# Optimization experiments

Hardware: AMD Instinct MI355X
Metric: run time of the kernel (lower is better)

## Reference

```python
import jax, jax.numpy as jnp
import numpy as np

NUM_HEADS = 8
ROPE_BASE = 10000.0


def _rope_cache(T, D, dtype=jnp.float32):
    # LLaMA-style rope cache: cos/sin of shape [T, D]
    inv_freq = 1.0 / (ROPE_BASE ** (jnp.arange(0, D, 2, dtype=dtype) / D))
    t = jnp.arange(T, dtype=dtype)
    freqs = t[:, None] * inv_freq[None, :]            # [T, D/2]
    emb = jnp.concatenate([freqs, freqs], axis=-1)    # [T, D]
    return jnp.cos(emb), jnp.sin(emb)


def _rotate_half(x):
    x1, x2 = jnp.split(x, 2, axis=-1)
    return jnp.concatenate([-x2, x1], axis=-1)


def setup_inputs() -> dict:
    key = jax.random.key(0)
    k1, k2, k3 = jax.random.split(key, 3)
    B, T, C = 4, 2048, 512
    x = jax.random.normal(k1, (B, T, C), dtype=jnp.float32)
    Wqkv = jax.random.normal(k2, (C, 3 * C), dtype=jnp.float32) * (1.0 / np.sqrt(C))
    Wproj = jax.random.normal(k3, (C, C), dtype=jnp.float32) * (1.0 / np.sqrt(C))
    return {"x": x, "Wqkv": Wqkv, "Wproj": Wproj}


def reference(x, Wqkv, Wproj):
    B, T, C = x.shape
    H = NUM_HEADS
    D = C // H

    qkv = jnp.einsum('btc,cf->btf', x, Wqkv)          # [B,T,3C]
    qkv = qkv.reshape(B, T, H, 3 * D)
    q, k, v = jnp.split(qkv, 3, axis=-1)              # each [B,T,H,D]
    q = q.transpose(0, 2, 1, 3)                       # [B,H,T,D]
    k = k.transpose(0, 2, 1, 3)
    v = v.transpose(0, 2, 1, 3)

    cos, sin = _rope_cache(T, D, dtype=x.dtype)       # [T,D]
    cos = cos[None, None, :, :]
    sin = sin[None, None, :, :]
    q = q * cos + _rotate_half(q) * sin
    k = k * cos + _rotate_half(k) * sin

    scale = 1.0 / np.sqrt(D)
    scores = jnp.einsum('bhqd,bhkd->bhqk', q, k) * scale  # [B,H,T,T]
    causal = jnp.tril(jnp.ones((T, T), dtype=bool))
    scores = jnp.where(causal[None, None, :, :], scores, jnp.finfo(scores.dtype).min)
    attn = jax.nn.softmax(scores, axis=-1)
    out = jnp.einsum('bhqk,bhkd->bhqd', attn, v)      # [B,H,T,D]
    out = out.transpose(0, 2, 1, 3).reshape(B, T, C)
    return jnp.einsum('btc,cd->btd', out, Wproj)
```

## Files before the change

kernel.cpp:

```cpp
#include <hip/hip_runtime.h>
#include <hip/hip_bf16.h>
#include <stdint.h>

constexpr int Bn = 4;
constexpr int Tn = 2048;
constexpr int Cn = 512;
constexpr int Hn = 8;
constexpr int Dn = 64;
constexpr int BT = Bn * Tn;
constexpr int NQKV = 3 * Cn;

typedef __attribute__((ext_vector_type(4))) float  f32x4;
typedef __attribute__((ext_vector_type(8))) short  s16x8;
typedef __attribute__((ext_vector_type(4))) short  s16x4;

__device__ __forceinline__ short f2bs(float f) {
    __hip_bfloat16 h = __float2bfloat16(f);
    return *reinterpret_cast<short*>(&h);
}

__device__ __forceinline__ void gload16(const short* g, short* l) {
    __builtin_amdgcn_global_load_lds(
        (const __attribute__((address_space(1))) void*)g,
        (__attribute__((address_space(3))) void*)l, 16, 0, 0);
}


__global__ __launch_bounds__(256) void k_conv_x(const float* __restrict__ x,
                                                short* __restrict__ xb) {
    int i = blockIdx.x * 256 + threadIdx.x;
    f32x4 v = reinterpret_cast<const f32x4*>(x)[i];
    s16x4 o;
    o[0] = f2bs(v[0]); o[1] = f2bs(v[1]); o[2] = f2bs(v[2]); o[3] = f2bs(v[3]);
    reinterpret_cast<s16x4*>(xb)[i] = o;
}

__global__ __launch_bounds__(256) void k_wTt(const float* __restrict__ Wqkv,
                                             const float* __restrict__ Wproj,
                                             short* __restrict__ wqkvT,
                                             short* __restrict__ wprojT) {
    int bid = blockIdx.x;
    const float* W; short* out; int N, n0, k0;
    if (bid < 192) {
        W = Wqkv; out = wqkvT; N = NQKV;
        n0 = (bid >> 3) * 64; k0 = (bid & 7) * 64;
    } else {
        bid -= 192;
        W = Wproj; out = wprojT; N = Cn;
        n0 = (bid >> 3) * 64; k0 = (bid & 7) * 64;
    }
    __shared__ float lds[64 * 65];
    const int tid = threadIdx.x;
#pragma unroll
    for (int i = 0; i < 16; ++i) {
        int flat = i * 256 + tid;
        int k = flat >> 6, n = flat & 63;
        lds[n * 65 + k] = W[(size_t)(k0 + k) * N + n0 + n];
    }
    __syncthreads();
#pragma unroll
    for (int i = 0; i < 16; ++i) {
        int flat = i * 256 + tid;
        int n = flat >> 6, k = flat & 63;
        out[(size_t)(n0 + n) * 512 + k0 + k] = f2bs(lds[n * 65 + k]);
    }
}

__global__ __launch_bounds__(256) void k_rope(float2* __restrict__ csT) {
    int i = blockIdx.x * 256 + threadIdx.x;
    int t = i >> 6, d = i & 63;
    float inv = exp2f(-(float)(d & 31) * 0.41524101186f);
    float fr = (float)t * inv;
    csT[i] = make_float2(cosf(fr), sinf(fr));
}


template <int MODE>
__global__ __launch_bounds__(256, 2) void gemm_kernel(
    const short* __restrict__ A, const short* __restrict__ Bt,
    const float2* __restrict__ csT,
    short* __restrict__ Qb, short* __restrict__ Kb, short* __restrict__ Vt,
    float* __restrict__ outF) {
    const int m0 = blockIdx.y * 128;
    const int n0 = blockIdx.x * 128;
    const int tid = threadIdx.x;
    const int w = tid >> 6, lane = tid & 63;
    const int qi = lane & 15, g = lane >> 4;
    const int wr = w >> 1, wc = w & 1;

    __shared__ short As[2][128 * 64];
    __shared__ short Bs[2][128 * 64];

    f32x4 acc[4][4];
#pragma unroll
    for (int mt = 0; mt < 4; ++mt)
#pragma unroll
        for (int nt = 0; nt < 4; ++nt) acc[mt][nt] = (f32x4){0.f, 0.f, 0.f, 0.f};

    const int lr = lane >> 3;
    const int lc = (lane & 7) ^ lr;

#define STAGEG(buf, k0)                                                         \
    {                                                                           \
        _Pragma("unroll")                                                       \
        for (int s4_ = 0; s4_ < 4; ++s4_) {                                     \
            int slot_ = s4_ * 4 + w;                                            \
            int r_ = slot_ * 8 + lr;                                            \
            gload16(&A[(size_t)(m0 + r_) * 512 + (k0) + lc * 8],                \
                    &As[buf][slot_ * 512 + lane * 8]);                          \
            gload16(&Bt[(size_t)(n0 + r_) * 512 + (k0) + lc * 8],               \
                    &Bs[buf][slot_ * 512 + lane * 8]);                          \
        }                                                                       \
    }

    STAGEG(0, 0);
    __syncthreads();

    for (int it = 0; it < 8; ++it) {
        if (it + 1 < 8) STAGEG((it + 1) & 1, (it + 1) * 64);
        const int cur = it & 1;
#pragma unroll
        for (int kk = 0; kk < 2; ++kk) {
            s16x8 af[4], bf[4];
#pragma unroll
            for (int mt = 0; mt < 4; ++mt) {
                int row = wr * 64 + mt * 16 + qi;
                af[mt] = *(const s16x8*)&As[cur][row * 64 + (((kk << 2) | g) ^ (qi & 7)) * 8];
            }
#pragma unroll
            for (int nt = 0; nt < 4; ++nt) {
                int row = wc * 64 + nt * 16 + qi;
                bf[nt] = *(const s16x8*)&Bs[cur][row * 64 + (((kk << 2) | g) ^ (qi & 7)) * 8];
            }
#pragma unroll
            for (int mt = 0; mt < 4; ++mt)
#pragma unroll
                for (int nt = 0; nt < 4; ++nt)
                    acc[mt][nt] = __builtin_amdgcn_mfma_f32_16x16x32_bf16(
                        af[mt], bf[nt], acc[mt][nt], 0, 0, 0);
        }
        __syncthreads();
    }
#undef STAGEG

    if (MODE == 1) {
#pragma unroll
        for (int mt = 0; mt < 4; ++mt)
#pragma unroll
            for (int nt = 0; nt < 4; ++nt)
#pragma unroll
                for (int r = 0; r < 4; ++r)
                    outF[(size_t)(m0 + wr * 64 + mt * 16 + 4 * g + r) * 512 +
                         n0 + wc * 64 + nt * 16 + qi] = acc[mt][nt][r];
    } else {
        const int seg64 = (n0 >> 6) + wc;
        const int h = seg64 / 3;
        const int seg = seg64 % 3;
        const int b = m0 >> 11;
        const int tb = (m0 & 2047) + wr * 64;
        const float QSC = 0.125f * 1.44269504f;
        if (seg == 2) {
            const size_t vbase = (size_t)(b * Hn + h) * Dn;
#pragma unroll
            for (int mt = 0; mt < 4; ++mt)
#pragma unroll
                for (int nt = 0; nt < 4; ++nt)
#pragma unroll
                    for (int r = 0; r < 4; ++r) {
                        int t = tb + mt * 16 + 4 * g + r;
                        int d = nt * 16 + qi;
                        int o = t & 31;
                        int jj = (t & ~31) + ((o >> 2) & 3) * 8 + (o >> 4) * 4 + (o & 3);
                        Vt[(vbase + d) * Tn + jj] = f2bs(acc[mt][nt][r]);
                    }
        } else {
            short* dst = (seg == 0) ? Qb : Kb;
            const float post = (seg == 0) ? QSC : 1.0f;
            const size_t headbase = (size_t)(b * Hn + h) * Tn;
#pragma unroll
            for (int mt = 0; mt < 4; ++mt)
#pragma unroll
                for (int nt = 0; nt < 4; ++nt)
#pragma unroll
                    for (int r = 0; r < 4; ++r) {
                        int t = tb + mt * 16 + 4 * g + r;
                        int d = nt * 16 + qi;
                        float val = acc[mt][nt][r];
                        float pv = (nt < 2) ? -acc[mt][nt + 2][r] : acc[mt][nt - 2][r];
                        float2 cs = csT[t * 64 + d];
                        dst[(headbase + t) * Dn + d] = f2bs((val * cs.x + pv * cs.y) * post);
                    }
        }
    }
}


__global__ __launch_bounds__(256, 4) void attn_kernel(const short* __restrict__ Qb,
                                                      const short* __restrict__ Kb,
                                                      const short* __restrict__ Vt,
                                                      short* __restrict__ AO) {
    const int idx = blockIdx.x;
    const int bh = idx & 31;
    const int qt = 31 - (idx >> 5);
    const int q0 = qt * 64;
    const int tid = threadIdx.x;
    const int w = tid >> 6, lane = tid & 63;
    const int qi = lane & 15, g = lane >> 4;
    const int b = bh >> 3, h = bh & 7;

    __shared__ short Ks[2][64 * 64];
    __shared__ short Vs[2][64 * 64];

    const short* Qh = Qb + (size_t)bh * Tn * Dn;
    const short* Kh = Kb + (size_t)bh * Tn * Dn;
    const short* Vh = Vt + (size_t)bh * Dn * Tn;

    const int wrow0 = q0 + w * 16;
    s16x8 qf[2];
#pragma unroll
    for (int dh = 0; dh < 2; ++dh)
        qf[dh] = *(const s16x8*)&Qh[(size_t)(wrow0 + qi) * Dn + dh * 32 + g * 8];

    f32x4 O[4];
#pragma unroll
    for (int dt = 0; dt < 4; ++dt) O[dt] = (f32x4){0.f, 0.f, 0.f, 0.f};
    float lsum = 0.f;

    const int nch = qt + 1;
    const f32x4 z4 = {0.f, 0.f, 0.f, 0.f};

    const int lr = lane >> 3;
    const int lc = (lane & 7) ^ lr;

#define STAGE(buf, ch)                                                          \
    {                                                                           \
        const int kv0_ = (ch) * 64;                                             \
        _Pragma("unroll")                                                       \
        for (int i_ = 0; i_ < 2; ++i_) {                                        \
            int slot_ = i_ * 4 + w;                                             \
            int r_ = slot_ * 8 + lr;                                            \
            gload16(&Kh[(size_t)(kv0_ + r_) * 64 + lc * 8],                     \
                    &Ks[buf][slot_ * 512 + lane * 8]);                          \
            gload16(&Vh[(size_t)r_ * Tn + kv0_ + lc * 8],                       \
                    &Vs[buf][slot_ * 512 + lane * 8]);                          \
        }                                                                       \
    }

    STAGE(0, 0);
    __syncthreads();

    for (int ch = 0; ch < nch; ++ch) {
        if (ch + 1 < nch) STAGE((ch + 1) & 1, ch + 1);
        const int kv0 = ch * 64;
        const int cur = ch & 1;

        f32x4 sacc[4];
#pragma unroll
        for (int sub = 0; sub < 4; ++sub) {
            const int krow = sub * 16 + qi;
            s16x8 ka = *(const s16x8*)&Ks[cur][krow * 64 + ((g ^ (qi & 7))) * 8];
            s16x8 kc = *(const s16x8*)&Ks[cur][krow * 64 + (((4 | g) ^ (qi & 7))) * 8];
            f32x4 t0 = __builtin_amdgcn_mfma_f32_16x16x32_bf16(ka, qf[0], z4, 0, 0, 0);
            sacc[sub] = __builtin_amdgcn_mfma_f32_16x16x32_bf16(kc, qf[1], t0, 0, 0, 0);
        }

        float pe[16];
        if (kv0 + 63 <= wrow0) {
#pragma unroll
            for (int e2 = 0; e2 < 16; ++e2)
                pe[e2] = exp2f(sacc[e2 >> 2][e2 & 3]);
        } else {
            const int qrow = wrow0 + qi;
#pragma unroll
            for (int sub = 0; sub < 4; ++sub)
#pragma unroll
                for (int r = 0; r < 4; ++r) {
                    int key = kv0 + sub * 16 + 4 * g + r;
                    pe[sub * 4 + r] = (key <= qrow) ? exp2f(sacc[sub][r]) : 0.f;
                }
        }
        {
            float a0 = (pe[0] + pe[1]) + (pe[2] + pe[3]);
            float a1 = (pe[4] + pe[5]) + (pe[6] + pe[7]);
            float a2 = (pe[8] + pe[9]) + (pe[10] + pe[11]);
            float a3 = (pe[12] + pe[13]) + (pe[14] + pe[15]);
            lsum += (a0 + a1) + (a2 + a3);
        }
        s16x8 pf[2];
#pragma unroll
        for (int c = 0; c < 2; ++c)
#pragma unroll
            for (int e2 = 0; e2 < 8; ++e2) pf[c][e2] = f2bs(pe[c * 8 + e2]);

#pragma unroll
        for (int c = 0; c < 2; ++c)
#pragma unroll
            for (int dt = 0; dt < 4; ++dt) {
                const int vrow = dt * 16 + qi;
                s16x8 vf = *(const s16x8*)&Vs[cur][vrow * 64 +
                                                   ((((c << 2) | g) ^ (qi & 7))) * 8];
                O[dt] = __builtin_amdgcn_mfma_f32_16x16x32_bf16(
                    pf[c], vf, O[dt], 0, 0, 0);
            }
        __syncthreads();
    }
#undef STAGE

    lsum += __shfl_xor(lsum, 16);
    lsum += __shfl_xor(lsum, 32);

#pragma unroll
    for (int r = 0; r < 4; ++r) {
        float li = __shfl(lsum, 4 * g + r);
        float inv = 1.f / li;
        int t = wrow0 + 4 * g + r;
#pragma unroll
        for (int dt = 0; dt < 4; ++dt)
            AO[((size_t)(b * Tn + t)) * Cn + h * 64 + dt * 16 + qi] =
                f2bs(O[dt][r] * inv);
    }
}


extern "C" void kernel_launch(void* const* d_in, const int* in_sizes, int n_in,
                              void* d_out, int out_size, void* d_ws, size_t ws_size,
                              hipStream_t stream) {
    const float* x = (const float*)d_in[0];
    const float* Wqkv = (const float*)d_in[1];
    const float* Wproj = (const float*)d_in[2];
    float* out = (float*)d_out;

    char* ws = (char*)d_ws;
    size_t o = 0;
    short* xb = (short*)(ws + o);      o += (size_t)BT * Cn * 2;
    short* wqkvT = (short*)(ws + o);   o += (size_t)NQKV * Cn * 2;
    short* wprojT = (short*)(ws + o);  o += (size_t)Cn * Cn * 2;
    short* Qb = (short*)(ws + o);      o += (size_t)Bn * Hn * Tn * Dn * 2;
    short* Kb = (short*)(ws + o);      o += (size_t)Bn * Hn * Tn * Dn * 2;
    short* Vt = (short*)(ws + o);      o += (size_t)Bn * Hn * Tn * Dn * 2;
    float2* csT = (float2*)(ws + o);   o += (size_t)Tn * Dn * 8;

    k_conv_x<<<BT * Cn / 4 / 256, 256, 0, stream>>>(x, xb);
    k_wTt<<<dim3(256), 256, 0, stream>>>(Wqkv, Wproj, wqkvT, wprojT);
    k_rope<<<Tn * Dn / 256, 256, 0, stream>>>(csT);

    gemm_kernel<0><<<dim3(NQKV / 128, BT / 128), 256, 0, stream>>>(
        xb, wqkvT, csT, Qb, Kb, Vt, nullptr);

    attn_kernel<<<dim3(1024), 256, 0, stream>>>(Qb, Kb, Vt, xb );

    gemm_kernel<1><<<dim3(Cn / 128, BT / 128), 256, 0, stream>>>(
        xb , wprojT, csT, nullptr, nullptr, nullptr, out);
}
```

Baseline: 93.73 us.

## Split KV chunks across warp pairs, with 32 query rows per warp and LDS reduction

The attention kernel now gives each warp 32 query rows, two 16-row subtiles, instead of 16. The four warps are split into two parity groups that handle alternating KV chunks. Each loaded K/V fragment from LDS is reused for two MFMAs, and warps skip chunks that lie fully past the causal diagonal of their rows. At the end, partial O accumulators and row sums from the odd-parity warps are reduced through shared memory before normalisation. This cuts LDS reads per MFMA and skips masked work, at the cost of more registers, half the warps idling on each chunk, and an extra reduction step.

```diff
diff --git a/kernel.cpp b/kernel.cpp
--- a/kernel.cpp
+++ b/kernel.cpp
@@ -206,6 +206,8 @@
     const int tid = threadIdx.x;
     const int w = tid >> 6, lane = tid & 63;
     const int qi = lane & 15, g = lane >> 4;
+    const int p = w & 1;
+    const int par = w >> 1;
     const int b = bh >> 3, h = bh & 7;
 
     __shared__ short Ks[2][64 * 64];
@@ -215,16 +217,21 @@
     const short* Kh = Kb + (size_t)bh * Tn * Dn;
     const short* Vh = Vt + (size_t)bh * Dn * Tn;
 
-    const int wrow0 = q0 + w * 16;
-    s16x8 qf[2];
-#pragma unroll
-    for (int dh = 0; dh < 2; ++dh)
-        qf[dh] = *(const s16x8*)&Qh[(size_t)(wrow0 + qi) * Dn + dh * 32 + g * 8];
-
-    f32x4 O[4];
-#pragma unroll
-    for (int dt = 0; dt < 4; ++dt) O[dt] = (f32x4){0.f, 0.f, 0.f, 0.f};
-    float lsum = 0.f;
+    const int wrow0 = q0 + p * 32;
+    s16x8 qf[2][2];
+#pragma unroll
+    for (int qs = 0; qs < 2; ++qs)
+#pragma unroll
+        for (int dh = 0; dh < 2; ++dh)
+            qf[qs][dh] = *(const s16x8*)&Qh[(size_t)(wrow0 + qs * 16 + qi) * Dn +
+                                            dh * 32 + g * 8];
+
+    f32x4 O[2][4];
+#pragma unroll
+    for (int qs = 0; qs < 2; ++qs)
+#pragma unroll
+        for (int dt = 0; dt < 4; ++dt) O[qs][dt] = (f32x4){0.f, 0.f, 0.f, 0.f};
+    float lsum[2] = {0.f, 0.f};
 
     const int nch = qt + 1;
     const f32x4 z4 = {0.f, 0.f, 0.f, 0.f};
@@ -254,70 +261,109 @@
         const int kv0 = ch * 64;
         const int cur = ch & 1;
 
-        f32x4 sacc[4];
-#pragma unroll
-        for (int sub = 0; sub < 4; ++sub) {
-            const int krow = sub * 16 + qi;
-            s16x8 ka = *(const s16x8*)&Ks[cur][krow * 64 + ((g ^ (qi & 7))) * 8];
-            s16x8 kc = *(const s16x8*)&Ks[cur][krow * 64 + (((4 | g) ^ (qi & 7))) * 8];
-            f32x4 t0 = __builtin_amdgcn_mfma_f32_16x16x32_bf16(ka, qf[0], z4, 0, 0, 0);
-            sacc[sub] = __builtin_amdgcn_mfma_f32_16x16x32_bf16(kc, qf[1], t0, 0, 0, 0);
-        }
-
-        float pe[16];
-        if (kv0 + 63 <= wrow0) {
-#pragma unroll
-            for (int e2 = 0; e2 < 16; ++e2)
-                pe[e2] = exp2f(sacc[e2 >> 2][e2 & 3]);
-        } else {
-            const int qrow = wrow0 + qi;
-#pragma unroll
-            for (int sub = 0; sub < 4; ++sub)
-#pragma unroll
-                for (int r = 0; r < 4; ++r) {
-                    int key = kv0 + sub * 16 + 4 * g + r;
-                    pe[sub * 4 + r] = (key <= qrow) ? exp2f(sacc[sub][r]) : 0.f;
+        if ((ch & 1) == par && kv0 <= wrow0 + 31) {
+            f32x4 sacc[2][4];
+#pragma unroll
+            for (int sub = 0; sub < 4; ++sub) {
+                const int krow = sub * 16 + qi;
+                s16x8 ka = *(const s16x8*)&Ks[cur][krow * 64 + ((g ^ (qi & 7))) * 8];
+                s16x8 kc = *(const s16x8*)&Ks[cur][krow * 64 + (((4 | g) ^ (qi & 7))) * 8];
+#pragma unroll
+                for (int qs = 0; qs < 2; ++qs) {
+                    f32x4 t0 = __builtin_amdgcn_mfma_f32_16x16x32_bf16(ka, qf[qs][0], z4, 0, 0, 0);
+                    sacc[qs][sub] = __builtin_amdgcn_mfma_f32_16x16x32_bf16(kc, qf[qs][1], t0, 0, 0, 0);
+                }
+            }
+
+            s16x8 pf[2][2];
+#pragma unroll
+            for (int qs = 0; qs < 2; ++qs) {
+                const int qsbase = wrow0 + qs * 16;
+                const int qrow = qsbase + qi;
+                float pe[16];
+                if (kv0 + 63 <= qsbase) {
+#pragma unroll
+                    for (int e2 = 0; e2 < 16; ++e2)
+                        pe[e2] = exp2f(sacc[qs][e2 >> 2][e2 & 3]);
+                } else {
+#pragma unroll
+                    for (int sub = 0; sub < 4; ++sub)
+#pragma unroll
+                        for (int r = 0; r < 4; ++r) {
+                            int key = kv0 + sub * 16 + 4 * g + r;
+                            pe[sub * 4 + r] = (key <= qrow) ? exp2f(sacc[qs][sub][r]) : 0.f;
+                        }
+                }
+                {
+                    float a0 = (pe[0] + pe[1]) + (pe[2] + pe[3]);
+                    float a1 = (pe[4] + pe[5]) + (pe[6] + pe[7]);
+                    float a2 = (pe[8] + pe[9]) + (pe[10] + pe[11]);
+                    float a3 = (pe[12] + pe[13]) + (pe[14] + pe[15]);
+                    lsum[qs] += (a0 + a1) + (a2 + a3);
+                }
+#pragma unroll
+                for (int c = 0; c < 2; ++c)
+#pragma unroll
+                    for (int e2 = 0; e2 < 8; ++e2) pf[qs][c][e2] = f2bs(pe[c * 8 + e2]);
+            }
+
+#pragma unroll
+            for (int c = 0; c < 2; ++c)
+#pragma unroll
+                for (int dt = 0; dt < 4; ++dt) {
+                    const int vrow = dt * 16 + qi;
+                    s16x8 vf = *(const s16x8*)&Vs[cur][vrow * 64 +
+                                                       ((((c << 2) | g) ^ (qi & 7))) * 8];
+#pragma unroll
+                    for (int qs = 0; qs < 2; ++qs)
+                        O[qs][dt] = __builtin_amdgcn_mfma_f32_16x16x32_bf16(
+                            pf[qs][c], vf, O[qs][dt], 0, 0, 0);
                 }
         }
-        {
-            float a0 = (pe[0] + pe[1]) + (pe[2] + pe[3]);
-            float a1 = (pe[4] + pe[5]) + (pe[6] + pe[7]);
-            float a2 = (pe[8] + pe[9]) + (pe[10] + pe[11]);
-            float a3 = (pe[12] + pe[13]) + (pe[14] + pe[15]);
-            lsum += (a0 + a1) + (a2 + a3);
+        __syncthreads();
+    }
+#undef STAGE
+
+    lsum[0] += __shfl_xor(lsum[0], 16); lsum[0] += __shfl_xor(lsum[0], 32);
+    lsum[1] += __shfl_xor(lsum[1], 16); lsum[1] += __shfl_xor(lsum[1], 32);
+
+    f32x4* Of4 = (f32x4*)&Ks[0][0];
+    float* Lf = (float*)&Vs[0][0];
+    if (w >= 2) {
+#pragma unroll
+        for (int qs = 0; qs < 2; ++qs)
+#pragma unroll
+            for (int dt = 0; dt < 4; ++dt)
+                Of4[(p * 64 + lane) * 8 + ((qs * 4 + dt) ^ (lane & 7))] = O[qs][dt];
+        if (g == 0) {
+            Lf[p * 32 + qi] = lsum[0];
+            Lf[p * 32 + 16 + qi] = lsum[1];
         }
-        s16x8 pf[2];
-#pragma unroll
-        for (int c = 0; c < 2; ++c)
-#pragma unroll
-            for (int e2 = 0; e2 < 8; ++e2) pf[c][e2] = f2bs(pe[c * 8 + e2]);
-
-#pragma unroll
-        for (int c = 0; c < 2; ++c)
+    }
+    __syncthreads();
+    if (w < 2) {
+        float lt[2];
+        lt[0] = lsum[0] + Lf[p * 32 + qi];
+        lt[1] = lsum[1] + Lf[p * 32 + 16 + qi];
+#pragma unroll
+        for (int qs = 0; qs < 2; ++qs) {
 #pragma unroll
             for (int dt = 0; dt < 4; ++dt) {
-                const int vrow = dt * 16 + qi;
-                s16x8 vf = *(const s16x8*)&Vs[cur][vrow * 64 +
-                                                   ((((c << 2) | g) ^ (qi & 7))) * 8];
-                O[dt] = __builtin_amdgcn_mfma_f32_16x16x32_bf16(
-                    pf[c], vf, O[dt], 0, 0, 0);
-            }
-        __syncthreads();
-    }
-#undef STAGE
-
-    lsum += __shfl_xor(lsum, 16);
-    lsum += __shfl_xor(lsum, 32);
-
-#pragma unroll
-    for (int r = 0; r < 4; ++r) {
-        float li = __shfl(lsum, 4 * g + r);
-        float inv = 1.f / li;
-        int t = wrow0 + 4 * g + r;
-#pragma unroll
-        for (int dt = 0; dt < 4; ++dt)
-            AO[((size_t)(b * Tn + t)) * Cn + h * 64 + dt * 16 + qi] =
-                f2bs(O[dt][r] * inv);
+                f32x4 part = Of4[(p * 64 + lane) * 8 + ((qs * 4 + dt) ^ (lane & 7))];
+                O[qs][dt][0] += part[0]; O[qs][dt][1] += part[1];
+                O[qs][dt][2] += part[2]; O[qs][dt][3] += part[3];
+            }
+#pragma unroll
+            for (int r = 0; r < 4; ++r) {
+                float li = __shfl(lt[qs], 4 * g + r);
+                float inv = 1.f / li;
+                int t = wrow0 + qs * 16 + 4 * g + r;
+#pragma unroll
+                for (int dt = 0; dt < 4; ++dt)
+                    AO[((size_t)(b * Tn + t)) * Cn + h * 64 + dt * 16 + qi] =
+                        f2bs(O[qs][dt][r] * inv);
+            }
+        }
     }
 }
 
```

Result: slower. 121.1 us (+29.2%).

## Split long causal attention query tiles across two blocks and combine partials

Applied to the files above, without the earlier changes.

Query tiles 16-31 now have their key chunks split into two ranges, each processed by a separate block via a lookup table that orders the work units by size. The partial unnormalized outputs and row sums go to a workspace, and a new combine kernel adds them and normalizes. Causal chunks a warp does not need are also skipped per warp. The goal is better load balance, with no long tail of big blocks. The cost is an extra kernel launch and an fp32 partial round trip through global memory. There is no max subtraction, so combining by plain addition stays consistent with the existing softmax.

```diff
diff --git a/kernel.cpp b/kernel.cpp
--- a/kernel.cpp
+++ b/kernel.cpp
@@ -24,6 +24,20 @@
         (const __attribute__((address_space(1))) void*)g,
         (__attribute__((address_space(3))) void*)l, 16, 0, 0);
 }
+
+__device__ const uint32_t UT[48] = {
+    (31u<<16)|(0u<<8)|16u, (31u<<16)|(16u<<8)|32u, (30u<<16)|(15u<<8)|31u, (15u<<16)|(0u<<8)|16u,
+    (30u<<16)|(0u<<8)|15u, (29u<<16)|(0u<<8)|15u, (29u<<16)|(15u<<8)|30u, (28u<<16)|(14u<<8)|29u, (14u<<16)|(0u<<8)|15u,
+    (28u<<16)|(0u<<8)|14u, (27u<<16)|(0u<<8)|14u, (27u<<16)|(14u<<8)|28u, (26u<<16)|(13u<<8)|27u, (13u<<16)|(0u<<8)|14u,
+    (26u<<16)|(0u<<8)|13u, (25u<<16)|(0u<<8)|13u, (25u<<16)|(13u<<8)|26u, (24u<<16)|(12u<<8)|25u, (12u<<16)|(0u<<8)|13u,
+    (24u<<16)|(0u<<8)|12u, (23u<<16)|(0u<<8)|12u, (23u<<16)|(12u<<8)|24u, (22u<<16)|(11u<<8)|23u, (11u<<16)|(0u<<8)|12u,
+    (22u<<16)|(0u<<8)|11u, (21u<<16)|(0u<<8)|11u, (21u<<16)|(11u<<8)|22u, (20u<<16)|(10u<<8)|21u, (10u<<16)|(0u<<8)|11u,
+    (20u<<16)|(0u<<8)|10u, (19u<<16)|(0u<<8)|10u, (19u<<16)|(10u<<8)|20u, (18u<<16)|(9u<<8)|19u,  (9u<<16)|(0u<<8)|10u,
+    (18u<<16)|(0u<<8)|9u,  (17u<<16)|(0u<<8)|9u,  (17u<<16)|(9u<<8)|18u,  (16u<<16)|(8u<<8)|17u,  (8u<<16)|(0u<<8)|9u,
+    (16u<<16)|(0u<<8)|8u,  (7u<<16)|(0u<<8)|8u,
+    (6u<<16)|(0u<<8)|7u, (5u<<16)|(0u<<8)|6u, (4u<<16)|(0u<<8)|5u, (3u<<16)|(0u<<8)|4u,
+    (2u<<16)|(0u<<8)|3u, (1u<<16)|(0u<<8)|2u, (0u<<16)|(0u<<8)|1u
+};
 
 
 __global__ __launch_bounds__(256) void k_conv_x(const float* __restrict__ x,
@@ -198,10 +212,14 @@
 __global__ __launch_bounds__(256, 4) void attn_kernel(const short* __restrict__ Qb,
                                                       const short* __restrict__ Kb,
                                                       const short* __restrict__ Vt,
-                                                      short* __restrict__ AO) {
+                                                      short* __restrict__ AO,
+                                                      float* __restrict__ Opart,
+                                                      float* __restrict__ Lpart) {
     const int idx = blockIdx.x;
     const int bh = idx & 31;
-    const int qt = 31 - (idx >> 5);
+    const uint32_t e = UT[idx >> 5];
+    const int qt = e >> 16;
+    const int chlo = (e >> 8) & 255, chhi = e & 255;
     const int q0 = qt * 64;
     const int tid = threadIdx.x;
     const int w = tid >> 6, lane = tid & 63;
@@ -226,7 +244,6 @@
     for (int dt = 0; dt < 4; ++dt) O[dt] = (f32x4){0.f, 0.f, 0.f, 0.f};
     float lsum = 0.f;
 
-    const int nch = qt + 1;
     const f32x4 z4 = {0.f, 0.f, 0.f, 0.f};
 
     const int lr = lane >> 3;
@@ -246,62 +263,65 @@
         }                                                                       \
     }
 
-    STAGE(0, 0);
+    STAGE(0, chlo);
     __syncthreads();
 
-    for (int ch = 0; ch < nch; ++ch) {
-        if (ch + 1 < nch) STAGE((ch + 1) & 1, ch + 1);
+    for (int ch = chlo; ch < chhi; ++ch) {
+        const int rel = ch - chlo;
+        if (ch + 1 < chhi) STAGE((rel + 1) & 1, ch + 1);
         const int kv0 = ch * 64;
-        const int cur = ch & 1;
-
-        f32x4 sacc[4];
-#pragma unroll
-        for (int sub = 0; sub < 4; ++sub) {
-            const int krow = sub * 16 + qi;
-            s16x8 ka = *(const s16x8*)&Ks[cur][krow * 64 + ((g ^ (qi & 7))) * 8];
-            s16x8 kc = *(const s16x8*)&Ks[cur][krow * 64 + (((4 | g) ^ (qi & 7))) * 8];
-            f32x4 t0 = __builtin_amdgcn_mfma_f32_16x16x32_bf16(ka, qf[0], z4, 0, 0, 0);
-            sacc[sub] = __builtin_amdgcn_mfma_f32_16x16x32_bf16(kc, qf[1], t0, 0, 0, 0);
-        }
-
-        float pe[16];
-        if (kv0 + 63 <= wrow0) {
-#pragma unroll
-            for (int e2 = 0; e2 < 16; ++e2)
-                pe[e2] = exp2f(sacc[e2 >> 2][e2 & 3]);
-        } else {
-            const int qrow = wrow0 + qi;
-#pragma unroll
-            for (int sub = 0; sub < 4; ++sub)
-#pragma unroll
-                for (int r = 0; r < 4; ++r) {
-                    int key = kv0 + sub * 16 + 4 * g + r;
-                    pe[sub * 4 + r] = (key <= qrow) ? exp2f(sacc[sub][r]) : 0.f;
+        const int cur = rel & 1;
+
+        if (kv0 <= wrow0 + 15) {
+            f32x4 sacc[4];
+#pragma unroll
+            for (int sub = 0; sub < 4; ++sub) {
+                const int krow = sub * 16 + qi;
+                s16x8 ka = *(const s16x8*)&Ks[cur][krow * 64 + ((g ^ (qi & 7))) * 8];
+                s16x8 kc = *(const s16x8*)&Ks[cur][krow * 64 + (((4 | g) ^ (qi & 7))) * 8];
+                f32x4 t0 = __builtin_amdgcn_mfma_f32_16x16x32_bf16(ka, qf[0], z4, 0, 0, 0);
+                sacc[sub] = __builtin_amdgcn_mfma_f32_16x16x32_bf16(kc, qf[1], t0, 0, 0, 0);
+            }
+
+            float pe[16];
+            if (kv0 + 63 <= wrow0) {
+#pragma unroll
+                for (int e2 = 0; e2 < 16; ++e2)
+                    pe[e2] = exp2f(sacc[e2 >> 2][e2 & 3]);
+            } else {
+                const int qrow = wrow0 + qi;
+#pragma unroll
+                for (int sub = 0; sub < 4; ++sub)
+#pragma unroll
+                    for (int r = 0; r < 4; ++r) {
+                        int key = kv0 + sub * 16 + 4 * g + r;
+                        pe[sub * 4 + r] = (key <= qrow) ? exp2f(sacc[sub][r]) : 0.f;
+                    }
+            }
+            {
+                float a0 = (pe[0] + pe[1]) + (pe[2] + pe[3]);
+                float a1 = (pe[4] + pe[5]) + (pe[6] + pe[7]);
+                float a2 = (pe[8] + pe[9]) + (pe[10] + pe[11]);
+                float a3 = (pe[12] + pe[13]) + (pe[14] + pe[15]);
+                lsum += (a0 + a1) + (a2 + a3);
+            }
+            s16x8 pf[2];
+#pragma unroll
+            for (int c = 0; c < 2; ++c)
+#pragma unroll
+                for (int e2 = 0; e2 < 8; ++e2) pf[c][e2] = f2bs(pe[c * 8 + e2]);
+
+#pragma unroll
+            for (int c = 0; c < 2; ++c)
+#pragma unroll
+                for (int dt = 0; dt < 4; ++dt) {
+                    const int vrow = dt * 16 + qi;
+                    s16x8 vf = *(const s16x8*)&Vs[cur][vrow * 64 +
+                                                       ((((c << 2) | g) ^ (qi & 7))) * 8];
+                    O[dt] = __builtin_amdgcn_mfma_f32_16x16x32_bf16(
+                        pf[c], vf, O[dt], 0, 0, 0);
                 }
         }
-        {
-            float a0 = (pe[0] + pe[1]) + (pe[2] + pe[3]);
-            float a1 = (pe[4] + pe[5]) + (pe[6] + pe[7]);
-            float a2 = (pe[8] + pe[9]) + (pe[10] + pe[11]);
-            float a3 = (pe[12] + pe[13]) + (pe[14] + pe[15]);
-            lsum += (a0 + a1) + (a2 + a3);
-        }
-        s16x8 pf[2];
-#pragma unroll
-        for (int c = 0; c < 2; ++c)
-#pragma unroll
-            for (int e2 = 0; e2 < 8; ++e2) pf[c][e2] = f2bs(pe[c * 8 + e2]);
-
-#pragma unroll
-        for (int c = 0; c < 2; ++c)
-#pragma unroll
-            for (int dt = 0; dt < 4; ++dt) {
-                const int vrow = dt * 16 + qi;
-                s16x8 vf = *(const s16x8*)&Vs[cur][vrow * 64 +
-                                                   ((((c << 2) | g) ^ (qi & 7))) * 8];
-                O[dt] = __builtin_amdgcn_mfma_f32_16x16x32_bf16(
-                    pf[c], vf, O[dt], 0, 0, 0);
-            }
         __syncthreads();
     }
 #undef STAGE
@@ -309,16 +329,57 @@
     lsum += __shfl_xor(lsum, 16);
     lsum += __shfl_xor(lsum, 32);
 
-#pragma unroll
-    for (int r = 0; r < 4; ++r) {
-        float li = __shfl(lsum, 4 * g + r);
-        float inv = 1.f / li;
-        int t = wrow0 + 4 * g + r;
-#pragma unroll
-        for (int dt = 0; dt < 4; ++dt)
-            AO[((size_t)(b * Tn + t)) * Cn + h * 64 + dt * 16 + qi] =
-                f2bs(O[dt][r] * inv);
-    }
+    if (qt < 16) {
+#pragma unroll
+        for (int r = 0; r < 4; ++r) {
+            float li = __shfl(lsum, 4 * g + r);
+            float inv = 1.f / li;
+            int t = wrow0 + 4 * g + r;
+#pragma unroll
+            for (int dt = 0; dt < 4; ++dt)
+                AO[((size_t)(b * Tn + t)) * Cn + h * 64 + dt * 16 + qi] =
+                    f2bs(O[dt][r] * inv);
+        }
+    } else {
+        const int pu = (bh * 16 + (qt - 16)) * 2 + (chlo ? 1 : 0);
+        float* Op = Opart + (size_t)pu * 4096;
+        if (g == 0) Lpart[pu * 64 + w * 16 + qi] = lsum;
+#pragma unroll
+        for (int r = 0; r < 4; ++r) {
+            int lrow = w * 16 + 4 * g + r;
+#pragma unroll
+            for (int dt = 0; dt < 4; ++dt)
+                Op[lrow * 64 + dt * 16 + qi] = O[dt][r];
+        }
+    }
+}
+
+
+__global__ __launch_bounds__(256) void combine_kernel(const float* __restrict__ Opart,
+                                                      const float* __restrict__ Lpart,
+                                                      short* __restrict__ AO) {
+    const int u = blockIdx.x;
+    const int bh = u & 31, sqt = u >> 5;
+    const int pu = (bh * 16 + sqt) * 2;
+    const int row = threadIdx.x >> 2;
+    const int d0 = (threadIdx.x & 3) * 16;
+
+    const float* O0 = Opart + (size_t)pu * 4096 + row * 64 + d0;
+    const float* O1 = O0 + 4096;
+    float l = Lpart[pu * 64 + row] + Lpart[(pu + 1) * 64 + row];
+    float inv = 1.f / l;
+
+    const int b = bh >> 3, h = bh & 7;
+    const int t = (16 + sqt) * 64 + row;
+    short* dst = &AO[((size_t)(b * Tn + t)) * Cn + h * 64 + d0];
+
+    s16x8 ov;
+#pragma unroll
+    for (int j = 0; j < 8; ++j) ov[j] = f2bs((O0[j] + O1[j]) * inv);
+    *(s16x8*)dst = ov;
+#pragma unroll
+    for (int j = 0; j < 8; ++j) ov[j] = f2bs((O0[8 + j] + O1[8 + j]) * inv);
+    *(s16x8*)(dst + 8) = ov;
 }
 
 
@@ -339,6 +400,8 @@
     short* Kb = (short*)(ws + o);      o += (size_t)Bn * Hn * Tn * Dn * 2;
     short* Vt = (short*)(ws + o);      o += (size_t)Bn * Hn * Tn * Dn * 2;
     float2* csT = (float2*)(ws + o);   o += (size_t)Tn * Dn * 8;
+    float* Opart = (float*)(ws + o);   o += (size_t)512 * 2 * 4096 * 4;
+    float* Lpart = (float*)(ws + o);   o += (size_t)512 * 2 * 64 * 4;
 
     k_conv_x<<<BT * Cn / 4 / 256, 256, 0, stream>>>(x, xb);
     k_wTt<<<dim3(256), 256, 0, stream>>>(Wqkv, Wproj, wqkvT, wprojT);
@@ -347,7 +410,10 @@
     gemm_kernel<0><<<dim3(NQKV / 128, BT / 128), 256, 0, stream>>>(
         xb, wqkvT, csT, Qb, Kb, Vt, nullptr);
 
-    attn_kernel<<<dim3(1024), 256, 0, stream>>>(Qb, Kb, Vt, xb );
+    attn_kernel<<<dim3(48 * 32), 256, 0, stream>>>(Qb, Kb, Vt, xb ,
+                                                   Opart, Lpart);
+
+    combine_kernel<<<dim3(512), 256, 0, stream>>>(Opart, Lpart, xb );
 
     gemm_kernel<1><<<dim3(Cn / 128, BT / 128), 256, 0, stream>>>(
         xb , wprojT, csT, nullptr, nullptr, nullptr, out);
```

New measurement: 95.93 us. +2.3%, slower.

## Merge prep kernels, load V fragments directly from global, skip masked-out chunks

Applied to the files above, without the earlier changes.

Folds the three preprocessing kernels (x conversion, weight transpose, rope table) into one launch, saving two kernel launches and their gaps. In attention, V is no longer staged into shared memory: each lane reads its V^T fragments straight from global memory, which halves the LDS footprint and the async copy traffic. Warps whose query rows lie entirely before the current key chunk now skip the score, softmax and PV work for that chunk. The trade-off is that V reads become uncoalesced global loads on the critical path with no prefetch. The merged prep kernel also reserves shared memory in every block, including blocks that do not use it.

```diff
diff --git a/kernel.cpp b/kernel.cpp
--- a/kernel.cpp
+++ b/kernel.cpp
@@ -26,52 +26,54 @@
 }
 
 
-__global__ __launch_bounds__(256) void k_conv_x(const float* __restrict__ x,
-                                                short* __restrict__ xb) {
-    int i = blockIdx.x * 256 + threadIdx.x;
-    f32x4 v = reinterpret_cast<const f32x4*>(x)[i];
-    s16x4 o;
-    o[0] = f2bs(v[0]); o[1] = f2bs(v[1]); o[2] = f2bs(v[2]); o[3] = f2bs(v[3]);
-    reinterpret_cast<s16x4*>(xb)[i] = o;
-}
-
-__global__ __launch_bounds__(256) void k_wTt(const float* __restrict__ Wqkv,
-                                             const float* __restrict__ Wproj,
-                                             short* __restrict__ wqkvT,
-                                             short* __restrict__ wprojT) {
-    int bid = blockIdx.x;
-    const float* W; short* out; int N, n0, k0;
-    if (bid < 192) {
-        W = Wqkv; out = wqkvT; N = NQKV;
-        n0 = (bid >> 3) * 64; k0 = (bid & 7) * 64;
+__global__ __launch_bounds__(256) void k_prep(const float* __restrict__ x,
+                                              const float* __restrict__ Wqkv,
+                                              const float* __restrict__ Wproj,
+                                              short* __restrict__ xb,
+                                              short* __restrict__ wqkvT,
+                                              short* __restrict__ wprojT,
+                                              float2* __restrict__ csT) {
+    const int bid = blockIdx.x;
+    const int tid = threadIdx.x;
+    __shared__ float lds[64 * 65];
+
+    if (bid < 4096) {
+        int i = bid * 256 + tid;
+        f32x4 v = reinterpret_cast<const f32x4*>(x)[i];
+        s16x4 o;
+        o[0] = f2bs(v[0]); o[1] = f2bs(v[1]); o[2] = f2bs(v[2]); o[3] = f2bs(v[3]);
+        reinterpret_cast<s16x4*>(xb)[i] = o;
+    } else if (bid < 4352) {
+        int wb = bid - 4096;
+        const float* W; short* out; int N, n0, k0;
+        if (wb < 192) {
+            W = Wqkv; out = wqkvT; N = NQKV;
+            n0 = (wb >> 3) * 64; k0 = (wb & 7) * 64;
+        } else {
+            wb -= 192;
+            W = Wproj; out = wprojT; N = Cn;
+            n0 = (wb >> 3) * 64; k0 = (wb & 7) * 64;
+        }
+#pragma unroll
+        for (int i = 0; i < 16; ++i) {
+            int flat = i * 256 + tid;
+            int k = flat >> 6, n = flat & 63;
+            lds[n * 65 + k] = W[(size_t)(k0 + k) * N + n0 + n];
+        }
+        __syncthreads();
+#pragma unroll
+        for (int i = 0; i < 16; ++i) {
+            int flat = i * 256 + tid;
+            int n = flat >> 6, k = flat & 63;
+            out[(size_t)(n0 + n) * 512 + k0 + k] = f2bs(lds[n * 65 + k]);
+        }
     } else {
-        bid -= 192;
-        W = Wproj; out = wprojT; N = Cn;
-        n0 = (bid >> 3) * 64; k0 = (bid & 7) * 64;
-    }
-    __shared__ float lds[64 * 65];
-    const int tid = threadIdx.x;
-#pragma unroll
-    for (int i = 0; i < 16; ++i) {
-        int flat = i * 256 + tid;
-        int k = flat >> 6, n = flat & 63;
-        lds[n * 65 + k] = W[(size_t)(k0 + k) * N + n0 + n];
-    }
-    __syncthreads();
-#pragma unroll
-    for (int i = 0; i < 16; ++i) {
-        int flat = i * 256 + tid;
-        int n = flat >> 6, k = flat & 63;
-        out[(size_t)(n0 + n) * 512 + k0 + k] = f2bs(lds[n * 65 + k]);
-    }
-}
-
-__global__ __launch_bounds__(256) void k_rope(float2* __restrict__ csT) {
-    int i = blockIdx.x * 256 + threadIdx.x;
-    int t = i >> 6, d = i & 63;
-    float inv = exp2f(-(float)(d & 31) * 0.41524101186f);
-    float fr = (float)t * inv;
-    csT[i] = make_float2(cosf(fr), sinf(fr));
+        int i = (bid - 4352) * 256 + tid;
+        int t = i >> 6, d = i & 63;
+        float inv = exp2f(-(float)(d & 31) * 0.41524101186f);
+        float fr = (float)t * inv;
+        csT[i] = make_float2(cosf(fr), sinf(fr));
+    }
 }
 
 
@@ -209,7 +211,6 @@
     const int b = bh >> 3, h = bh & 7;
 
     __shared__ short Ks[2][64 * 64];
-    __shared__ short Vs[2][64 * 64];
 
     const short* Qh = Qb + (size_t)bh * Tn * Dn;
     const short* Kh = Kb + (size_t)bh * Tn * Dn;
@@ -241,8 +242,6 @@
             int r_ = slot_ * 8 + lr;                                            \
             gload16(&Kh[(size_t)(kv0_ + r_) * 64 + lc * 8],                     \
                     &Ks[buf][slot_ * 512 + lane * 8]);                          \
-            gload16(&Vh[(size_t)r_ * Tn + kv0_ + lc * 8],                       \
-                    &Vs[buf][slot_ * 512 + lane * 8]);                          \
         }                                                                       \
     }
 
@@ -254,54 +253,60 @@
         const int kv0 = ch * 64;
         const int cur = ch & 1;
 
-        f32x4 sacc[4];
-#pragma unroll
-        for (int sub = 0; sub < 4; ++sub) {
-            const int krow = sub * 16 + qi;
-            s16x8 ka = *(const s16x8*)&Ks[cur][krow * 64 + ((g ^ (qi & 7))) * 8];
-            s16x8 kc = *(const s16x8*)&Ks[cur][krow * 64 + (((4 | g) ^ (qi & 7))) * 8];
-            f32x4 t0 = __builtin_amdgcn_mfma_f32_16x16x32_bf16(ka, qf[0], z4, 0, 0, 0);
-            sacc[sub] = __builtin_amdgcn_mfma_f32_16x16x32_bf16(kc, qf[1], t0, 0, 0, 0);
-        }
-
-        float pe[16];
-        if (kv0 + 63 <= wrow0) {
-#pragma unroll
-            for (int e2 = 0; e2 < 16; ++e2)
-                pe[e2] = exp2f(sacc[e2 >> 2][e2 & 3]);
-        } else {
-            const int qrow = wrow0 + qi;
-#pragma unroll
-            for (int sub = 0; sub < 4; ++sub)
-#pragma unroll
-                for (int r = 0; r < 4; ++r) {
-                    int key = kv0 + sub * 16 + 4 * g + r;
-                    pe[sub * 4 + r] = (key <= qrow) ? exp2f(sacc[sub][r]) : 0.f;
-                }
-        }
-        {
-            float a0 = (pe[0] + pe[1]) + (pe[2] + pe[3]);
-            float a1 = (pe[4] + pe[5]) + (pe[6] + pe[7]);
-            float a2 = (pe[8] + pe[9]) + (pe[10] + pe[11]);
-            float a3 = (pe[12] + pe[13]) + (pe[14] + pe[15]);
-            lsum += (a0 + a1) + (a2 + a3);
-        }
-        s16x8 pf[2];
-#pragma unroll
-        for (int c = 0; c < 2; ++c)
-#pragma unroll
-            for (int e2 = 0; e2 < 8; ++e2) pf[c][e2] = f2bs(pe[c * 8 + e2]);
-
-#pragma unroll
-        for (int c = 0; c < 2; ++c)
-#pragma unroll
-            for (int dt = 0; dt < 4; ++dt) {
-                const int vrow = dt * 16 + qi;
-                s16x8 vf = *(const s16x8*)&Vs[cur][vrow * 64 +
-                                                   ((((c << 2) | g) ^ (qi & 7))) * 8];
-                O[dt] = __builtin_amdgcn_mfma_f32_16x16x32_bf16(
-                    pf[c], vf, O[dt], 0, 0, 0);
-            }
+        if (kv0 <= wrow0 + 15) {
+            f32x4 sacc[4];
+#pragma unroll
+            for (int sub = 0; sub < 4; ++sub) {
+                const int krow = sub * 16 + qi;
+                s16x8 ka = *(const s16x8*)&Ks[cur][krow * 64 + ((g ^ (qi & 7))) * 8];
+                s16x8 kc = *(const s16x8*)&Ks[cur][krow * 64 + (((4 | g) ^ (qi & 7))) * 8];
+                f32x4 t0 = __builtin_amdgcn_mfma_f32_16x16x32_bf16(ka, qf[0], z4, 0, 0, 0);
+                sacc[sub] = __builtin_amdgcn_mfma_f32_16x16x32_bf16(kc, qf[1], t0, 0, 0, 0);
+            }
+
+            s16x8 vf[2][4];
+#pragma unroll
+            for (int c = 0; c < 2; ++c)
+#pragma unroll
+                for (int dt = 0; dt < 4; ++dt)
+                    vf[c][dt] = *(const s16x8*)&Vh[(size_t)(dt * 16 + qi) * Tn +
+                                                   kv0 + c * 32 + g * 8];
+
+            float pe[16];
+            if (kv0 + 63 <= wrow0) {
+#pragma unroll
+                for (int e2 = 0; e2 < 16; ++e2)
+                    pe[e2] = exp2f(sacc[e2 >> 2][e2 & 3]);
+            } else {
+                const int qrow = wrow0 + qi;
+#pragma unroll
+                for (int sub = 0; sub < 4; ++sub)
+#pragma unroll
+                    for (int r = 0; r < 4; ++r) {
+                        int key = kv0 + sub * 16 + 4 * g + r;
+                        pe[sub * 4 + r] = (key <= qrow) ? exp2f(sacc[sub][r]) : 0.f;
+                    }
+            }
+            {
+                float a0 = (pe[0] + pe[1]) + (pe[2] + pe[3]);
+                float a1 = (pe[4] + pe[5]) + (pe[6] + pe[7]);
+                float a2 = (pe[8] + pe[9]) + (pe[10] + pe[11]);
+                float a3 = (pe[12] + pe[13]) + (pe[14] + pe[15]);
+                lsum += (a0 + a1) + (a2 + a3);
+            }
+            s16x8 pf[2];
+#pragma unroll
+            for (int c = 0; c < 2; ++c)
+#pragma unroll
+                for (int e2 = 0; e2 < 8; ++e2) pf[c][e2] = f2bs(pe[c * 8 + e2]);
+
+#pragma unroll
+            for (int c = 0; c < 2; ++c)
+#pragma unroll
+                for (int dt = 0; dt < 4; ++dt)
+                    O[dt] = __builtin_amdgcn_mfma_f32_16x16x32_bf16(
+                        pf[c], vf[c][dt], O[dt], 0, 0, 0);
+        }
         __syncthreads();
     }
 #undef STAGE
@@ -340,9 +345,7 @@
     short* Vt = (short*)(ws + o);      o += (size_t)Bn * Hn * Tn * Dn * 2;
     float2* csT = (float2*)(ws + o);   o += (size_t)Tn * Dn * 8;
 
-    k_conv_x<<<BT * Cn / 4 / 256, 256, 0, stream>>>(x, xb);
-    k_wTt<<<dim3(256), 256, 0, stream>>>(Wqkv, Wproj, wqkvT, wprojT);
-    k_rope<<<Tn * Dn / 256, 256, 0, stream>>>(csT);
+    k_prep<<<dim3(4864), 256, 0, stream>>>(x, Wqkv, Wproj, xb, wqkvT, wprojT, csT);
 
     gemm_kernel<0><<<dim3(NQKV / 128, BT / 128), 256, 0, stream>>>(
         xb, wqkvT, csT, Qb, Kb, Vt, nullptr);
```

Measured after the change: 136.3 us. +45.4%, slower.
